# Kernel tuning notes

Measured on AMD Instinct MI355X. Metric: run time of the kernel, lower is better.

## Reference

```python
import jax, jax.numpy as jnp
import numpy as np

N, E, IN_F, EDGE_F, HID, S = 200000, 600000, 28, 4, 128, 20000
NUM_LAYERS = 4
L = NUM_LAYERS - 1
BN_EPS = 1e-5


def setup_inputs() -> dict:
    key = jax.random.key(0)
    ks = jax.random.split(key, 20)
    p = lambda k, shape: (jax.random.normal(k, shape, dtype=jnp.float32) * 0.1)
    return {
        'x': jax.random.normal(ks[0], (N, IN_F), dtype=jnp.float32),
        'edge_index': jax.random.randint(ks[1], (2, E), 0, N),
        'edge_attr': jax.random.normal(ks[2], (E, EDGE_F), dtype=jnp.float32),
        'edge_weight': jax.random.uniform(ks[3], (E,), dtype=jnp.float32),
        'node_mask': (jax.random.uniform(ks[4], (N,)) > 0.5).astype(jnp.float32),
        'subgraphs2nodes': jax.random.randint(ks[5], (N,), 0, S),
        # layer-1 params (in_features -> hidden)
        'be1_W1': p(ks[6], (EDGE_F, IN_F)), 'be1_b1': jnp.zeros((IN_F,), jnp.float32),
        'be1_W2': p(ks[7], (IN_F, IN_F)), 'be1_b2': jnp.zeros((IN_F,), jnp.float32),
        'm1_W1': p(ks[8], (IN_F, HID)), 'm1_b1': jnp.zeros((HID,), jnp.float32),
        'm1_W2': p(ks[9], (HID, HID)), 'm1_b2': jnp.zeros((HID,), jnp.float32),
        'bn1_g': jnp.ones((HID,), jnp.float32), 'bn1_b': jnp.zeros((HID,), jnp.float32),
        'eps1': jnp.zeros((), jnp.float32),
        # layers 2..NUM_LAYERS, stacked (hidden -> hidden)
        'beW1': p(ks[10], (L, EDGE_F, HID)), 'beb1': jnp.zeros((L, HID), jnp.float32),
        'beW2': p(ks[11], (L, HID, HID)), 'beb2': jnp.zeros((L, HID), jnp.float32),
        'mW1': p(ks[12], (L, HID, HID)), 'mb1': jnp.zeros((L, HID), jnp.float32),
        'mW2': p(ks[13], (L, HID, HID)), 'mb2': jnp.zeros((L, HID), jnp.float32),
        'bng': jnp.ones((L, HID), jnp.float32), 'bnb': jnp.zeros((L, HID), jnp.float32),
        'eps': jnp.zeros((L,), jnp.float32),
    }


def _mlp2(h, W1, b1, W2, b2):
    # Linear -> ReLU -> Linear
    return jnp.dot(jax.nn.relu(jnp.dot(h, W1) + b1), W2) + b2


def _gine(x, src, dst, edge_attr, edge_weight, eps,
          beW1, beb1, beW2, beb2, W1, b1, W2, b2, g, beta):
    # bond encoder on edge features
    e = _mlp2(edge_attr, beW1, beb1, beW2, beb2)            # [E, d]
    # message: relu(x_j + e_ij) * w_ij, aggregated at dst via scatter-add
    m = jax.nn.relu(x[src] + e) * edge_weight[:, None]      # [E, d]
    aggr = jax.ops.segment_sum(m, dst, num_segments=N)      # [N, d]
    h = (1.0 + eps) * x + aggr
    # node MLP: Linear,ReLU,Linear,BN(train mode),ReLU
    h = _mlp2(h, W1, b1, W2, b2)
    mu = jnp.mean(h, axis=0)
    var = jnp.mean((h - mu) ** 2, axis=0)
    h = (h - mu) * jax.lax.rsqrt(var + BN_EPS) * g + beta
    return jax.nn.relu(h)


def reference(x, edge_index, edge_attr, edge_weight, node_mask, subgraphs2nodes,
              be1_W1, be1_b1, be1_W2, be1_b2, m1_W1, m1_b1, m1_W2, m1_b2,
              bn1_g, bn1_b, eps1,
              beW1, beb1, beW2, beb2, mW1, mb1, mW2, mb2, bng, bnb, eps):
    src, dst = edge_index[0], edge_index[1]
    h = _gine(x, src, dst, edge_attr, edge_weight, eps1,
              be1_W1, be1_b1, be1_W2, be1_b2,
              m1_W1, m1_b1, m1_W2, m1_b2, bn1_g, bn1_b)
    for i in range(L):
        h_new = _gine(h, src, dst, edge_attr, edge_weight, eps[i],
                      beW1[i], beb1[i], beW2[i], beb2[i],
                      mW1[i], mb1[i], mW2[i], mb2[i], bng[i], bnb[i])
        h = h + h_new  # residual
    # float node_mask branch + global_add_pool over subgraphs2nodes
    h = h * node_mask[:, None]
    return jax.ops.segment_sum(h, subgraphs2nodes, num_segments=S)  # [S, HID]
```

## Files before the change

### kernel.cpp

```cpp
#include <hip/hip_runtime.h>
#include <hip/hip_bf16.h>


#define BNEPS 1e-5f
#define LDA 136
#define SCAN_NB 240

typedef __attribute__((ext_vector_type(8))) short bf16x8;
typedef __attribute__((ext_vector_type(8))) unsigned short u16x8;
typedef __attribute__((ext_vector_type(4))) float f32x4;

__device__ inline short f2bf(float f) {
    __hip_bfloat16 h = __float2bfloat16(f);
    return *reinterpret_cast<short*>(&h);
}
__device__ inline unsigned short f2bfu(float f) {
    __hip_bfloat16 h = __float2bfloat16(f);
    return *reinterpret_cast<unsigned short*>(&h);
}
__device__ inline float bf2f(unsigned short u) {
    union { unsigned int i; float f; } v; v.i = ((unsigned int)u) << 16; return v.f;
}

__global__ __launch_bounds__(256) void k_prep(
    const float* __restrict__ m1W2, const float* __restrict__ beW2,
    const float* __restrict__ mW1, const float* __restrict__ mW2,
    short* __restrict__ out)
{
    __shared__ float tileS[64][65];
    int b = blockIdx.x, mat = b >> 2, t = b & 3;
    const float* Wsrc;
    if (mat == 0) Wsrc = m1W2;
    else {
        int l = (mat - 1) / 3, which = (mat - 1) % 3;
        Wsrc = (which == 0) ? beW2 + (size_t)l * 16384
             : (which == 1) ? mW1 + (size_t)l * 16384
             :                mW2 + (size_t)l * 16384;
    }
    short* dst = out + (size_t)mat * 16384;
    int tr = (t >> 1) * 64, tc = (t & 1) * 64;
    for (int i = threadIdx.x; i < 4096; i += 256) {
        int r = i >> 6, c = i & 63;
        tileS[r][c] = Wsrc[(size_t)(tr + r) * 128 + (tc + c)];
    }
    __syncthreads();
    for (int i = threadIdx.x; i < 4096; i += 256) {
        int n = i >> 6, k = i & 63;
        dst[(size_t)(tc + n) * 128 + (tr + k)] = f2bf(tileS[k][n]);
    }
}

__global__ __launch_bounds__(256) void k_prep1(
    const float* __restrict__ W1, short* __restrict__ out)
{
    for (int i = threadIdx.x; i < 128 * 32; i += 256) {
        int n = i >> 5, k = i & 31;
        out[i] = (k < 28) ? f2bf(W1[(size_t)k * 128 + n]) : (short)0;
    }
}

__global__ __launch_bounds__(256) void k_prep28(
    const float* __restrict__ W2, short* __restrict__ out)
{
    for (int i = threadIdx.x; i < 32 * 32; i += 256) {
        int n = i >> 5, k = i & 31;
        out[i] = (n < 28 && k < 28) ? f2bf(W2[(size_t)k * 28 + n]) : (short)0;
    }
}

__global__ __launch_bounds__(256) void k_prepx(
    const float* __restrict__ x, unsigned short* __restrict__ xbf, int N)
{
    int total = N * 32;
    for (int i = blockIdx.x * 256 + threadIdx.x; i < total; i += gridDim.x * 256) {
        int n = i >> 5, c = i & 31;
        xbf[i] = (c < 28) ? f2bfu(x[(size_t)n * 28 + c]) : (unsigned short)0;
    }
}

__global__ __launch_bounds__(256) void k_count(
    const int* __restrict__ ei, int* __restrict__ counts, int E)
{
    for (int e = blockIdx.x * 256 + threadIdx.x; e < E; e += gridDim.x * 256)
        atomicAdd(&counts[ei[E + e]], 1);
}

__global__ __launch_bounds__(256) void k_count2(
    const int* __restrict__ s2n, const float* __restrict__ mask,
    int* __restrict__ counts2, int N)
{
    for (int n = blockIdx.x * 256 + threadIdx.x; n < N; n += gridDim.x * 256)
        if (mask[n] != 0.f) atomicAdd(&counts2[s2n[n]], 1);
}

__global__ __launch_bounds__(256) void k_scanA(
    const int* __restrict__ counts, int* __restrict__ bsum, int N, int seg)
{
    __shared__ int red[256];
    int b = blockIdx.x;
    int lo = b * seg, hi = min(lo + seg, N);
    int s = 0;
    for (int i = lo + threadIdx.x; i < hi; i += 256) s += counts[i];
    red[threadIdx.x] = s;
    __syncthreads();
    for (int d = 128; d > 0; d >>= 1) {
        if (threadIdx.x < d) red[threadIdx.x] += red[threadIdx.x + d];
        __syncthreads();
    }
    if (threadIdx.x == 0) bsum[b] = red[0];
}

__global__ __launch_bounds__(256) void k_scanB(
    int* __restrict__ bsum, int nb, int* __restrict__ offs, int N)
{
    __shared__ int sh[256];
    int v = (threadIdx.x < nb) ? bsum[threadIdx.x] : 0;
    sh[threadIdx.x] = v;
    __syncthreads();
    for (int d = 1; d < 256; d <<= 1) {
        int t = (threadIdx.x >= d) ? sh[threadIdx.x - d] : 0;
        __syncthreads();
        sh[threadIdx.x] += t;
        __syncthreads();
    }
    if (threadIdx.x < nb) bsum[threadIdx.x] = sh[threadIdx.x] - v;
    if (threadIdx.x == 0) offs[N] = sh[255];
}

__global__ __launch_bounds__(256) void k_scanC(
    const int* __restrict__ counts, const int* __restrict__ bsum,
    int* __restrict__ offs, int* __restrict__ cursor, int N, int seg)
{
    __shared__ int sh[256];
    int b = blockIdx.x;
    int lo = b * seg, hi = min(lo + seg, N);
    int base = bsum[b];
    for (int t0 = lo; t0 < hi; t0 += 256) {
        int i = t0 + threadIdx.x;
        int v = (i < hi) ? counts[i] : 0;
        sh[threadIdx.x] = v;
        __syncthreads();
        for (int d = 1; d < 256; d <<= 1) {
            int t = (threadIdx.x >= d) ? sh[threadIdx.x - d] : 0;
            __syncthreads();
            sh[threadIdx.x] += t;
            __syncthreads();
        }
        int excl = base + sh[threadIdx.x] - v;
        if (i < hi) { offs[i] = excl; cursor[i] = excl; }
        int tileTotal = sh[255];
        __syncthreads();
        base += tileTotal;
    }
}

__global__ __launch_bounds__(256) void k_scatter(
    const int* __restrict__ ei, const float* __restrict__ ew,
    const float4* __restrict__ ea4,
    int* __restrict__ cursor, int2* __restrict__ pmeta,
    float4* __restrict__ pea4, int E)
{
    for (int e = blockIdx.x * 256 + threadIdx.x; e < E; e += gridDim.x * 256) {
        int d = ei[E + e];
        int pos = atomicAdd(&cursor[d], 1);
        pmeta[pos] = make_int2(ei[e], __float_as_int(ew[e]));
        pea4[pos] = ea4[e];
    }
}

__global__ __launch_bounds__(256) void k_scatter2(
    const int* __restrict__ s2n, const float* __restrict__ mask,
    int* __restrict__ cursor2, int* __restrict__ perm2, int N)
{
    for (int n = blockIdx.x * 256 + threadIdx.x; n < N; n += gridDim.x * 256)
        if (mask[n] != 0.f) {
            int pos = atomicAdd(&cursor2[s2n[n]], 1);
            perm2[pos] = n;
        }
}

__global__ __launch_bounds__(256) void k_emsg(
    const float4* __restrict__ pea4,
    const float* __restrict__ W1, const float* __restrict__ b1,
    const short* __restrict__ W2t, const float* __restrict__ b2,
    unsigned short* __restrict__ emsg, const int* __restrict__ offs,
    int n0, int n1)
{
    __shared__ short Bs[128 * LDA];
    __shared__ short As[64 * LDA];
    __shared__ float eas[64][4];
    int e0 = offs[n0], e1 = offs[n1];
    int tid = threadIdx.x;
    for (int i = tid; i < 2048; i += 256) {
        int n = (i * 8) >> 7, k = (i * 8) & 127;
        *(bf16x8*)&Bs[n * LDA + k] = *(const bf16x8*)&W2t[i * 8];
    }
    int j = tid & 127, half = tid >> 7;
    float w10 = W1[j], w11 = W1[128 + j], w12 = W1[256 + j], w13 = W1[384 + j];
    float b1j = b1[j];
    int w = tid >> 6, lane = tid & 63;
    int l15 = lane & 15, quad = lane >> 4;
    __syncthreads();

    int numTiles = (e1 - e0 + 63) >> 6;
    for (int tile = blockIdx.x; tile < numTiles; tile += gridDim.x) {
        int base = e0 + tile * 64;
        __syncthreads();
        if (tid < 64) {
            int k = base + tid;
            float4 a = make_float4(0.f, 0.f, 0.f, 0.f);
            if (k < e1) a = pea4[k];
            eas[tid][0] = a.x; eas[tid][1] = a.y; eas[tid][2] = a.z; eas[tid][3] = a.w;
        }
        __syncthreads();
        #pragma unroll
        for (int q = 0; q < 32; ++q) {
            int e = half * 32 + q;
            float t = fmaf(eas[e][0], w10, fmaf(eas[e][1], w11,
                      fmaf(eas[e][2], w12, fmaf(eas[e][3], w13, b1j))));
            As[e * LDA + j] = f2bf(fmaxf(t, 0.f));
        }
        __syncthreads();
        f32x4 acc[8];
        #pragma unroll
        for (int nt = 0; nt < 8; ++nt) acc[nt] = (f32x4){0.f, 0.f, 0.f, 0.f};
        #pragma unroll
        for (int kt = 0; kt < 4; ++kt) {
            bf16x8 af = *(bf16x8*)&As[(w * 16 + l15) * LDA + kt * 32 + quad * 8];
            #pragma unroll
            for (int nt = 0; nt < 8; ++nt) {
                bf16x8 bf = *(bf16x8*)&Bs[(nt * 16 + l15) * LDA + kt * 32 + quad * 8];
                acc[nt] = __builtin_amdgcn_mfma_f32_16x16x32_bf16(af, bf, acc[nt], 0, 0, 0);
            }
        }
        #pragma unroll
        for (int nt = 0; nt < 8; ++nt) {
            int col = nt * 16 + l15;
            float b2c = b2[col];
            #pragma unroll
            for (int r = 0; r < 4; ++r) {
                int row = w * 16 + quad * 4 + r;
                As[row * LDA + col] = f2bf(acc[nt][r] + b2c);
            }
        }
        __syncthreads();
        #pragma unroll
        for (int kk = 0; kk < 4; ++kk) {
            int i = tid + kk * 256;
            int row = (i * 8) >> 7, col = (i * 8) & 127;
            int gr = base + row;
            if (gr < e1)
                *(bf16x8*)&emsg[(size_t)(gr - e0) * 128 + col] = *(bf16x8*)&As[row * LDA + col];
        }
    }
}

__global__ __launch_bounds__(256) void k_emsg28_mm(
    const float4* __restrict__ pea4,
    const float* __restrict__ W1, const float* __restrict__ b1,
    const short* __restrict__ W2t28,
    const float* __restrict__ b2,
    unsigned short* __restrict__ emsg28, int E)
{
    __shared__ short Bs[32 * 40];
    __shared__ short As[64 * 40];
    __shared__ float eas[64][4];
    __shared__ float b2s[32];
    int tid = threadIdx.x;
    for (int i = tid; i < 32 * 32; i += 256) {
        int n = i >> 5, k = i & 31;
        Bs[n * 40 + k] = W2t28[i];
    }
    if (tid < 32) b2s[tid] = (tid < 28) ? b2[tid] : 0.f;
    int j = tid & 31, sub = tid >> 5;
    float w10 = 0.f, w11 = 0.f, w12 = 0.f, w13 = 0.f, b1j = 0.f;
    if (j < 28) { w10 = W1[j]; w11 = W1[28 + j]; w12 = W1[56 + j]; w13 = W1[84 + j]; b1j = b1[j]; }
    int w = tid >> 6, lane = tid & 63;
    int l15 = lane & 15, quad = lane >> 4;
    __syncthreads();

    int numTiles = (E + 63) >> 6;
    for (int tile = blockIdx.x; tile < numTiles; tile += gridDim.x) {
        int base = tile * 64;
        __syncthreads();
        if (tid < 64) {
            int k = base + tid;
            float4 a = (k < E) ? pea4[k] : make_float4(0.f, 0.f, 0.f, 0.f);
            eas[tid][0] = a.x; eas[tid][1] = a.y; eas[tid][2] = a.z; eas[tid][3] = a.w;
        }
        __syncthreads();
        #pragma unroll
        for (int q = 0; q < 8; ++q) {
            int e = q * 8 + sub;
            float t = fmaf(eas[e][0], w10, fmaf(eas[e][1], w11,
                      fmaf(eas[e][2], w12, fmaf(eas[e][3], w13, b1j))));
            As[e * 40 + j] = (j < 28) ? f2bf(fmaxf(t, 0.f)) : (short)0;
        }
        __syncthreads();
        f32x4 acc[2];
        acc[0] = (f32x4){0.f, 0.f, 0.f, 0.f};
        acc[1] = (f32x4){0.f, 0.f, 0.f, 0.f};
        bf16x8 af = *(bf16x8*)&As[(w * 16 + l15) * 40 + quad * 8];
        #pragma unroll
        for (int nt = 0; nt < 2; ++nt) {
            bf16x8 bf = *(bf16x8*)&Bs[(nt * 16 + l15) * 40 + quad * 8];
            acc[nt] = __builtin_amdgcn_mfma_f32_16x16x32_bf16(af, bf, acc[nt], 0, 0, 0);
        }
        __syncthreads();
        #pragma unroll
        for (int nt = 0; nt < 2; ++nt) {
            int col = nt * 16 + l15;
            float bb = b2s[col];
            #pragma unroll
            for (int r = 0; r < 4; ++r)
                As[(w * 16 + quad * 4 + r) * 40 + col] = f2bf(acc[nt][r] + bb);
        }
        __syncthreads();
        for (int i = tid; i < 64 * 28; i += 256) {
            int row = i / 28, col = i - row * 28;
            int gr = base + row;
            if (gr < E) emsg28[(size_t)gr * 28 + col] = As[row * 40 + col];
        }
    }
}

__global__ __launch_bounds__(256) void k_gather(
    const unsigned short* __restrict__ h, const int* __restrict__ offs,
    const int2* __restrict__ pmeta, const unsigned short* __restrict__ emsg,
    unsigned short* __restrict__ a0,
    const float* __restrict__ epsp, int epsIdx,
    int n0, int n1)
{
    int grp = threadIdx.x >> 5, lane = threadIdx.x & 31;
    int n = n0 + blockIdx.x * 8 + grp;
    if (n >= n1) return;
    int e0 = offs[n0];
    int k0 = offs[n], k1 = offs[n + 1];
    float s = 1.0f + epsp[epsIdx];
    ushort4 hv0 = *(const ushort4*)&h[(size_t)n * 128 + lane * 4];
    float m0 = s * bf2f(hv0.x), m1 = s * bf2f(hv0.y);
    float m2 = s * bf2f(hv0.z), m3 = s * bf2f(hv0.w);
    for (int k = k0; k < k1; ++k) {
        int2 mt = pmeta[k];
        float w = __int_as_float(mt.y);
        ushort4 ev = *(const ushort4*)&emsg[(size_t)(k - e0) * 128 + lane * 4];
        ushort4 hv = *(const ushort4*)&h[(size_t)mt.x * 128 + lane * 4];
        m0 += fmaxf(bf2f(hv.x) + bf2f(ev.x), 0.f) * w;
        m1 += fmaxf(bf2f(hv.y) + bf2f(ev.y), 0.f) * w;
        m2 += fmaxf(bf2f(hv.z) + bf2f(ev.z), 0.f) * w;
        m3 += fmaxf(bf2f(hv.w) + bf2f(ev.w), 0.f) * w;
    }
    ushort4 o;
    o.x = f2bfu(m0); o.y = f2bfu(m1); o.z = f2bfu(m2); o.w = f2bfu(m3);
    *(ushort4*)&a0[(size_t)n * 128 + lane * 4] = o;
}

__global__ __launch_bounds__(256) void k_gather28(
    const float* __restrict__ x, const unsigned short* __restrict__ xbf,
    const int* __restrict__ offs,
    const int2* __restrict__ pmeta, const unsigned short* __restrict__ emsg28,
    const float* __restrict__ eps1, float* __restrict__ u28, int N)
{
    int grp = threadIdx.x >> 5, lane = threadIdx.x & 31;
    int n = blockIdx.x * 8 + grp;
    if (n >= N || lane >= 28) return;
    float s = 1.0f + eps1[0];
    int k0 = offs[n], k1 = offs[n + 1];
    float m = 0.f;
    for (int k = k0; k < k1; ++k) {
        int2 mt = pmeta[k];
        float w = __int_as_float(mt.y);
        float e = bf2f(emsg28[(size_t)k * 28 + lane]);
        float xs = bf2f(xbf[(size_t)mt.x * 32 + lane]);
        m += fmaxf(xs + e, 0.f) * w;
    }
    u28[(size_t)n * 28 + lane] = fmaf(s, x[(size_t)n * 28 + lane], m);
}

__global__ __launch_bounds__(512) void k_mlp(
    const unsigned short* __restrict__ src, const short* __restrict__ Wt1,
    const float* __restrict__ b1, const short* __restrict__ Wt2,
    const float* __restrict__ b2, unsigned short* __restrict__ dst,
    float* __restrict__ stats, int N)
{
    __shared__ short Bs1[128 * LDA];
    __shared__ short Bs2[128 * LDA];
    __shared__ short As[128 * LDA];
    __shared__ float sstat[256];
    int tid = threadIdx.x;
    for (int i = tid; i < 2048; i += 512) {
        int n = (i * 8) >> 7, k = (i * 8) & 127;
        *(bf16x8*)&Bs1[n * LDA + k] = *(const bf16x8*)&Wt1[i * 8];
        *(bf16x8*)&Bs2[n * LDA + k] = *(const bf16x8*)&Wt2[i * 8];
    }
    if (tid < 256) sstat[tid] = 0.f;
    int w = tid >> 6, lane = tid & 63;
    int l15 = lane & 15, quad = lane >> 4;
    int cg = w >> 2;
    int rb = (w & 3) * 32;
    __syncthreads();

    bf16x8 B1f[4][4], B2f[4][4];
    float b1r[4], b2r[4];
    #pragma unroll
    for (int nt = 0; nt < 4; ++nt) {
        int col = cg * 64 + nt * 16 + l15;
        b1r[nt] = b1[col]; b2r[nt] = b2[col];
        #pragma unroll
        for (int kt = 0; kt < 4; ++kt) {
            B1f[nt][kt] = *(bf16x8*)&Bs1[col * LDA + kt * 32 + quad * 8];
            B2f[nt][kt] = *(bf16x8*)&Bs2[col * LDA + kt * 32 + quad * 8];
        }
    }
    float lsum[2][4], lsq[2][4];
    #pragma unroll
    for (int rg = 0; rg < 2; ++rg)
        #pragma unroll
        for (int nt = 0; nt < 4; ++nt) { lsum[rg][nt] = 0.f; lsq[rg][nt] = 0.f; }

    int numTiles = (N + 127) >> 7;
    for (int tile = blockIdx.x; tile < numTiles; tile += gridDim.x) {
        int base = tile * 128;
        __syncthreads();
        #pragma unroll
        for (int kk = 0; kk < 4; ++kk) {
            int i = tid + kk * 512;
            int row = (i * 8) >> 7, col = (i * 8) & 127;
            int rr = base + row;
            bf16x8 v;
            if (rr < N) v = *(const bf16x8*)&src[(size_t)rr * 128 + col];
            else        v = (bf16x8){0,0,0,0,0,0,0,0};
            *(bf16x8*)&As[row * LDA + col] = v;
        }
        __syncthreads();
        f32x4 acc[2][4];
        #pragma unroll
        for (int rg = 0; rg < 2; ++rg)
            #pragma unroll
            for (int nt = 0; nt < 4; ++nt) acc[rg][nt] = (f32x4){0.f, 0.f, 0.f, 0.f};
        #pragma unroll
        for (int rg = 0; rg < 2; ++rg) {
            #pragma unroll
            for (int kt = 0; kt < 4; ++kt) {
                bf16x8 af = *(bf16x8*)&As[(rb + rg * 16 + l15) * LDA + kt * 32 + quad * 8];
                #pragma unroll
                for (int nt = 0; nt < 4; ++nt)
                    acc[rg][nt] = __builtin_amdgcn_mfma_f32_16x16x32_bf16(af, B1f[nt][kt], acc[rg][nt], 0, 0, 0);
            }
        }
        __syncthreads();
        #pragma unroll
        for (int rg = 0; rg < 2; ++rg)
            #pragma unroll
            for (int nt = 0; nt < 4; ++nt) {
                int col = cg * 64 + nt * 16 + l15;
                #pragma unroll
                for (int r = 0; r < 4; ++r)
                    As[(rb + rg * 16 + quad * 4 + r) * LDA + col] =
                        f2bf(fmaxf(acc[rg][nt][r] + b1r[nt], 0.f));
            }
        __syncthreads();
        #pragma unroll
        for (int rg = 0; rg < 2; ++rg)
            #pragma unroll
            for (int nt = 0; nt < 4; ++nt) acc[rg][nt] = (f32x4){0.f, 0.f, 0.f, 0.f};
        #pragma unroll
        for (int rg = 0; rg < 2; ++rg) {
            #pragma unroll
            for (int kt = 0; kt < 4; ++kt) {
                bf16x8 af = *(bf16x8*)&As[(rb + rg * 16 + l15) * LDA + kt * 32 + quad * 8];
                #pragma unroll
                for (int nt = 0; nt < 4; ++nt)
                    acc[rg][nt] = __builtin_amdgcn_mfma_f32_16x16x32_bf16(af, B2f[nt][kt], acc[rg][nt], 0, 0, 0);
            }
        }
        __syncthreads();
        #pragma unroll
        for (int rg = 0; rg < 2; ++rg)
            #pragma unroll
            for (int nt = 0; nt < 4; ++nt) {
                int col = cg * 64 + nt * 16 + l15;
                int row0 = base + rb + rg * 16 + quad * 4;
                #pragma unroll
                for (int r = 0; r < 4; ++r) {
                    float z = acc[rg][nt][r] + b2r[nt];
                    if (row0 + r < N) { lsum[rg][nt] += z; lsq[rg][nt] = fmaf(z, z, lsq[rg][nt]); }
                    As[(rb + rg * 16 + quad * 4 + r) * LDA + col] = f2bf(z);
                }
            }
        __syncthreads();
        #pragma unroll
        for (int kk = 0; kk < 4; ++kk) {
            int i = tid + kk * 512;
            int row = (i * 8) >> 7, col = (i * 8) & 127;
            int rr = base + row;
            if (rr < N)
                *(bf16x8*)&dst[(size_t)rr * 128 + col] = *(bf16x8*)&As[row * LDA + col];
        }
    }
    #pragma unroll
    for (int nt = 0; nt < 4; ++nt) {
        int col = cg * 64 + nt * 16 + l15;
        atomicAdd(&sstat[col], lsum[0][nt] + lsum[1][nt]);
        atomicAdd(&sstat[128 + col], lsq[0][nt] + lsq[1][nt]);
    }
    __syncthreads();
    if (tid < 256) atomicAdd(&stats[tid], sstat[tid]);
}

__global__ __launch_bounds__(512) void k_mlp1(
    const float* __restrict__ u28, const short* __restrict__ Wt1p,
    const float* __restrict__ b1, const short* __restrict__ Wt2,
    const float* __restrict__ b2, unsigned short* __restrict__ dst,
    float* __restrict__ stats, int N)
{
    __shared__ short Bs1[128 * 40];
    __shared__ short Bs2[128 * LDA];
    __shared__ short As[128 * LDA];
    __shared__ short A28[128 * 40];
    __shared__ float sstat[256];
    int tid = threadIdx.x;
    for (int i = tid; i < 128 * 32; i += 512) {
        int n = i >> 5, k = i & 31;
        Bs1[n * 40 + k] = Wt1p[i];
    }
    for (int i = tid; i < 2048; i += 512) {
        int n = (i * 8) >> 7, k = (i * 8) & 127;
        *(bf16x8*)&Bs2[n * LDA + k] = *(const bf16x8*)&Wt2[i * 8];
    }
    {
        int r = tid >> 2, c = tid & 3;
        if (r < 128) A28[r * 40 + 28 + c] = 0;
    }
    if (tid < 256) sstat[tid] = 0.f;
    int w = tid >> 6, lane = tid & 63;
    int l15 = lane & 15, quad = lane >> 4;
    int cg = w >> 2, rb = (w & 3) * 32;
    __syncthreads();

    bf16x8 B1f[4], B2f[4][4];
    float b1r[4], b2r[4];
    #pragma unroll
    for (int nt = 0; nt < 4; ++nt) {
        int col = cg * 64 + nt * 16 + l15;
        b1r[nt] = b1[col]; b2r[nt] = b2[col];
        B1f[nt] = *(bf16x8*)&Bs1[col * 40 + quad * 8];
        #pragma unroll
        for (int kt = 0; kt < 4; ++kt)
            B2f[nt][kt] = *(bf16x8*)&Bs2[col * LDA + kt * 32 + quad * 8];
    }
    float lsum[2][4], lsq[2][4];
    #pragma unroll
    for (int rg = 0; rg < 2; ++rg)
        #pragma unroll
        for (int nt = 0; nt < 4; ++nt) { lsum[rg][nt] = 0.f; lsq[rg][nt] = 0.f; }

    int numTiles = (N + 127) >> 7;
    for (int tile = blockIdx.x; tile < numTiles; tile += gridDim.x) {
        int base = tile * 128;
        __syncthreads();
        for (int i = tid; i < 128 * 28; i += 512) {
            int row = i / 28, col = i - row * 28;
            int rr = base + row;
            A28[row * 40 + col] = (rr < N) ? f2bf(u28[(size_t)rr * 28 + col]) : (short)0;
        }
        __syncthreads();
        f32x4 acc[2][4];
        #pragma unroll
        for (int rg = 0; rg < 2; ++rg)
            #pragma unroll
            for (int nt = 0; nt < 4; ++nt) acc[rg][nt] = (f32x4){0.f, 0.f, 0.f, 0.f};
        #pragma unroll
        for (int rg = 0; rg < 2; ++rg) {
            bf16x8 af = *(bf16x8*)&A28[(rb + rg * 16 + l15) * 40 + quad * 8];
            #pragma unroll
            for (int nt = 0; nt < 4; ++nt)
                acc[rg][nt] = __builtin_amdgcn_mfma_f32_16x16x32_bf16(af, B1f[nt], acc[rg][nt], 0, 0, 0);
        }
        #pragma unroll
        for (int rg = 0; rg < 2; ++rg)
            #pragma unroll
            for (int nt = 0; nt < 4; ++nt) {
                int col = cg * 64 + nt * 16 + l15;
                #pragma unroll
                for (int r = 0; r < 4; ++r)
                    As[(rb + rg * 16 + quad * 4 + r) * LDA + col] =
                        f2bf(fmaxf(acc[rg][nt][r] + b1r[nt], 0.f));
            }
        __syncthreads();
        #pragma unroll
        for (int rg = 0; rg < 2; ++rg)
            #pragma unroll
            for (int nt = 0; nt < 4; ++nt) acc[rg][nt] = (f32x4){0.f, 0.f, 0.f, 0.f};
        #pragma unroll
        for (int rg = 0; rg < 2; ++rg) {
            #pragma unroll
            for (int kt = 0; kt < 4; ++kt) {
                bf16x8 af = *(bf16x8*)&As[(rb + rg * 16 + l15) * LDA + kt * 32 + quad * 8];
                #pragma unroll
                for (int nt = 0; nt < 4; ++nt)
                    acc[rg][nt] = __builtin_amdgcn_mfma_f32_16x16x32_bf16(af, B2f[nt][kt], acc[rg][nt], 0, 0, 0);
            }
        }
        __syncthreads();
        #pragma unroll
        for (int rg = 0; rg < 2; ++rg)
            #pragma unroll
            for (int nt = 0; nt < 4; ++nt) {
                int col = cg * 64 + nt * 16 + l15;
                int row0 = base + rb + rg * 16 + quad * 4;
                #pragma unroll
                for (int r = 0; r < 4; ++r) {
                    float z = acc[rg][nt][r] + b2r[nt];
                    if (row0 + r < N) { lsum[rg][nt] += z; lsq[rg][nt] = fmaf(z, z, lsq[rg][nt]); }
                    As[(rb + rg * 16 + quad * 4 + r) * LDA + col] = f2bf(z);
                }
            }
        __syncthreads();
        #pragma unroll
        for (int kk = 0; kk < 4; ++kk) {
            int i = tid + kk * 512;
            int row = (i * 8) >> 7, col = (i * 8) & 127;
            int rr = base + row;
            if (rr < N)
                *(bf16x8*)&dst[(size_t)rr * 128 + col] = *(bf16x8*)&As[row * LDA + col];
        }
    }
    #pragma unroll
    for (int nt = 0; nt < 4; ++nt) {
        int col = cg * 64 + nt * 16 + l15;
        atomicAdd(&sstat[col], lsum[0][nt] + lsum[1][nt]);
        atomicAdd(&sstat[128 + col], lsq[0][nt] + lsq[1][nt]);
    }
    __syncthreads();
    if (tid < 256) atomicAdd(&stats[tid], sstat[tid]);
}

__global__ __launch_bounds__(128) void k_stats(
    const float* __restrict__ stats, const float* __restrict__ g,
    const float* __restrict__ b, float* __restrict__ ss, float invN)
{
    int j = threadIdx.x;
    float mu  = stats[j] * invN;
    float var = fmaf(stats[128 + j], invN, -mu * mu);
    float sc  = rsqrtf(fmaxf(var, 0.f) + BNEPS) * g[j];
    ss[j] = sc;
    ss[128 + j] = fmaf(-mu, sc, b[j]);
}

__global__ __launch_bounds__(256) void k_bn(
    const unsigned short* __restrict__ z, const float* __restrict__ ss,
    unsigned short* __restrict__ h, int residual, int N)
{
    int idx8 = blockIdx.x * 256 + threadIdx.x;
    int stride = gridDim.x * 256;
    int c0 = (idx8 & 15) * 8;
    float scl[8], sht[8];
    #pragma unroll
    for (int r = 0; r < 8; ++r) { scl[r] = ss[c0 + r]; sht[r] = ss[128 + c0 + r]; }
    int total8 = N * 16;
    for (; idx8 < total8; idx8 += stride) {
        int n = idx8 >> 4;
        u16x8 z8 = *(const u16x8*)&z[(size_t)n * 128 + c0];
        float hn[8];
        #pragma unroll
        for (int r = 0; r < 8; ++r)
            hn[r] = fmaxf(fmaf(bf2f(z8[r]), scl[r], sht[r]), 0.f);
        if (residual) {
            u16x8 h8 = *(const u16x8*)&h[(size_t)n * 128 + c0];
            #pragma unroll
            for (int r = 0; r < 8; ++r) hn[r] += bf2f(h8[r]);
        }
        u16x8 o;
        #pragma unroll
        for (int r = 0; r < 8; ++r) o[r] = f2bfu(hn[r]);
        *(u16x8*)&h[(size_t)n * 128 + c0] = o;
    }
}

__global__ __launch_bounds__(256) void k_poolbn(
    const unsigned short* __restrict__ z, const unsigned short* __restrict__ hprev,
    const float* __restrict__ ss, const int* __restrict__ offs2,
    const int* __restrict__ perm2, float* __restrict__ out, int S)
{
    int w = threadIdx.x >> 6, lane = threadIdx.x & 63;
    int s = blockIdx.x * 4 + w;
    if (s >= S) return;
    int c0 = lane * 2;
    float scl0 = ss[c0], scl1 = ss[c0 + 1];
    float sht0 = ss[128 + c0], sht1 = ss[128 + c0 + 1];
    int k0 = offs2[s], k1 = offs2[s + 1];
    float a0 = 0.f, a1 = 0.f;
    for (int k = k0; k < k1; ++k) {
        int n = perm2[k];
        ushort2 zv = *(const ushort2*)&z[(size_t)n * 128 + c0];
        ushort2 hv = *(const ushort2*)&hprev[(size_t)n * 128 + c0];
        a0 += fmaxf(fmaf(bf2f(zv.x), scl0, sht0), 0.f) + bf2f(hv.x);
        a1 += fmaxf(fmaf(bf2f(zv.y), scl1, sht1), 0.f) + bf2f(hv.y);
    }
    *(float2*)&out[(size_t)s * 128 + c0] = make_float2(a0, a1);
}

extern "C" void kernel_launch(void* const* d_in, const int* in_sizes, int n_in,
                              void* d_out, int out_size, void* d_ws, size_t ws_size,
                              hipStream_t stream) {
    const float* x    = (const float*)d_in[0];
    const int*   ei   = (const int*)d_in[1];
    const float* ea   = (const float*)d_in[2];
    const float* ew   = (const float*)d_in[3];
    const float* mask = (const float*)d_in[4];
    const int*   s2n  = (const int*)d_in[5];
    const float* be1W1 = (const float*)d_in[6];
    const float* be1b1 = (const float*)d_in[7];
    const float* be1W2 = (const float*)d_in[8];
    const float* be1b2 = (const float*)d_in[9];
    const float* m1W1  = (const float*)d_in[10];
    const float* m1b1  = (const float*)d_in[11];
    const float* m1W2  = (const float*)d_in[12];
    const float* m1b2  = (const float*)d_in[13];
    const float* bn1g  = (const float*)d_in[14];
    const float* bn1b  = (const float*)d_in[15];
    const float* eps1  = (const float*)d_in[16];
    const float* beW1  = (const float*)d_in[17];
    const float* beb1  = (const float*)d_in[18];
    const float* beW2  = (const float*)d_in[19];
    const float* beb2  = (const float*)d_in[20];
    const float* mW1   = (const float*)d_in[21];
    const float* mb1   = (const float*)d_in[22];
    const float* mW2   = (const float*)d_in[23];
    const float* mb2   = (const float*)d_in[24];
    const float* bng   = (const float*)d_in[25];
    const float* bnb   = (const float*)d_in[26];
    const float* epsL  = (const float*)d_in[27];

    const int N = in_sizes[0] / 28;
    const int E = in_sizes[1] / 2;
    const int S = out_size / 128;
    const float invN = 1.0f / (float)N;
    const int NS = N / 2;
    const int EMC = E / 2 + 8192;

    auto al16 = [](size_t v) { return (v + 15) & ~(size_t)15; };
    char* ws = (char*)d_ws;
    size_t offH      = 0;
    size_t offA0     = al16(offH + (size_t)N * 256);
    size_t offEm     = al16(offA0 + (size_t)N * 256);
    size_t emBytes   = (size_t)EMC * 256;
    if ((size_t)E * 56 > emBytes) emBytes = (size_t)E * 56;
    size_t offStats  = al16(offEm + emBytes);
    size_t offSS     = al16(offStats + 4096);
    size_t offWts    = al16(offSS + 1024);
    size_t offCounts = al16(offWts + 10 * 16384 * 2 + 4096 * 2 + 1024 * 2);
    size_t offOffs   = al16(offCounts + (size_t)N * 4);
    size_t offCursor = al16(offOffs + (size_t)(N + 1) * 4);
    size_t offPmeta  = al16(offCursor + (size_t)N * 4);
    size_t offPea    = al16(offPmeta + (size_t)E * 8);
    size_t offBsum   = al16(offPea + (size_t)E * 16);
    size_t offCnt2   = al16(offBsum + SCAN_NB * 4);
    size_t offOffs2  = al16(offCnt2 + (size_t)S * 4);
    size_t offCur2   = al16(offOffs2 + (size_t)(S + 1) * 4);
    size_t offPerm2  = al16(offCur2 + (size_t)S * 4);
    size_t need      = offPerm2 + (size_t)N * 4;
    if (ws_size < need) return;

    unsigned short* h    = (unsigned short*)(ws + offH);
    unsigned short* a0   = (unsigned short*)(ws + offA0);
    unsigned short* emsg = (unsigned short*)(ws + offEm);
    float* u28    = (float*)(ws + offA0);
    unsigned short* xbf = (unsigned short*)(ws + offA0 + 26214400);
    float* stats  = (float*)(ws + offStats);
    float* ssbuf  = (float*)(ws + offSS);
    short* wts    = (short*)(ws + offWts);
    short* w1p    = wts + 10 * 16384;
    short* w2p28  = w1p + 4096;
    int*   counts = (int*)(ws + offCounts);
    int*   offs   = (int*)(ws + offOffs);
    int*   cursor = (int*)(ws + offCursor);
    int2*  pmeta  = (int2*)(ws + offPmeta);
    float4* pea4  = (float4*)(ws + offPea);
    int*   bsum   = (int*)(ws + offBsum);
    int*   cnt2   = (int*)(ws + offCnt2);
    int*   offs2  = (int*)(ws + offOffs2);
    int*   cur2   = (int*)(ws + offCur2);
    int*   perm2  = (int*)(ws + offPerm2);
    const float4* ea4 = (const float4*)ea;

    hipMemsetAsync(stats, 0, 4 * 256 * sizeof(float), stream);
    hipMemsetAsync(counts, 0, (size_t)N * sizeof(int), stream);
    hipMemsetAsync(cnt2, 0, (size_t)S * sizeof(int), stream);

    k_prep<<<40, 256, 0, stream>>>(m1W2, beW2, mW1, mW2, wts);
    k_prep1<<<1, 256, 0, stream>>>(m1W1, w1p);
    k_prep28<<<1, 256, 0, stream>>>(be1W2, w2p28);
    k_prepx<<<512, 256, 0, stream>>>(x, xbf, N);

    const int seg = (N + SCAN_NB - 1) / SCAN_NB;
    k_count<<<1024, 256, 0, stream>>>(ei, counts, E);
    k_scanA<<<SCAN_NB, 256, 0, stream>>>(counts, bsum, N, seg);
    k_scanB<<<1, 256, 0, stream>>>(bsum, SCAN_NB, offs, N);
    k_scanC<<<SCAN_NB, 256, 0, stream>>>(counts, bsum, offs, cursor, N, seg);
    k_scatter<<<1024, 256, 0, stream>>>(ei, ew, ea4, cursor, pmeta, pea4, E);

    const int seg2 = (S + SCAN_NB - 1) / SCAN_NB;
    k_count2<<<512, 256, 0, stream>>>(s2n, mask, cnt2, N);
    k_scanA<<<SCAN_NB, 256, 0, stream>>>(cnt2, bsum, S, seg2);
    k_scanB<<<1, 256, 0, stream>>>(bsum, SCAN_NB, offs2, S);
    k_scanC<<<SCAN_NB, 256, 0, stream>>>(cnt2, bsum, offs2, cur2, S, seg2);
    k_scatter2<<<512, 256, 0, stream>>>(s2n, mask, cur2, perm2, N);

    auto wt_be = [&](int l) { return wts + (size_t)(1 + 3 * l + 0) * 16384; };
    auto wt_m1 = [&](int l) { return wts + (size_t)(1 + 3 * l + 1) * 16384; };
    auto wt_m2 = [&](int l) { return wts + (size_t)(1 + 3 * l + 2) * 16384; };

    k_emsg28_mm<<<2048, 256, 0, stream>>>(pea4, be1W1, be1b1, w2p28, be1b2, emsg, E);
    k_gather28<<<(N + 7) / 8, 256, 0, stream>>>(x, xbf, offs, pmeta, emsg, eps1, u28, N);
    k_mlp1<<<512, 512, 0, stream>>>(u28, w1p, m1b1, wts , m1b2, h, stats, N);
    k_stats<<<1, 128, 0, stream>>>(stats, bn1g, bn1b, ssbuf, invN);
    k_bn<<<2048, 256, 0, stream>>>(h, ssbuf, h, 0, N);

    for (int l = 0; l < 3; ++l) {
        for (int c = 0; c < 2; ++c) {
            int n0 = (c == 0) ? 0 : NS;
            int n1 = (c == 0) ? NS : N;
            k_emsg<<<2048, 256, 0, stream>>>(pea4,
                beW1 + (size_t)l * 512, beb1 + (size_t)l * 128,
                wt_be(l), beb2 + (size_t)l * 128, emsg, offs, n0, n1);
            k_gather<<<(n1 - n0 + 7) / 8, 256, 0, stream>>>(h, offs, pmeta, emsg, a0,
                epsL, l, n0, n1);
        }
        k_mlp<<<512, 512, 0, stream>>>(a0, wt_m1(l), mb1 + (size_t)l * 128,
                                       wt_m2(l), mb2 + (size_t)l * 128, a0,
                                       stats + 256 * (l + 1), N);
        k_stats<<<1, 128, 0, stream>>>(stats + 256 * (l + 1),
            bng + (size_t)l * 128, bnb + (size_t)l * 128, ssbuf, invN);
        if (l < 2) {
            k_bn<<<2048, 256, 0, stream>>>(a0, ssbuf, h, 1, N);
        }
    }

    k_poolbn<<<(S + 3) / 4, 256, 0, stream>>>(a0, h, ssbuf, offs2, perm2,
                                              (float*)d_out, S);
}
```

Baseline: 1.041 ms.

## Stream MLP weight fragments from global/L2 instead of LDS and registers

Removes the shared-memory copies of the weight matrices in k_emsg, k_mlp and k_mlp1 and stops holding all weight fragments in registers. Each k-step now loads its B fragments straight from global memory, relying on L2/L1 caching. Launch bounds now request 4 blocks per CU. The goal is less LDS use and fewer registers so more blocks fit per CU, at the cost of repeated global loads of the weights on every tile.

Result: slower. 1.785 ms (+71.5%).

```diff
diff --git a/kernel.cpp b/kernel.cpp
--- a/kernel.cpp
+++ b/kernel.cpp
@@ -179,28 +179,23 @@
         }
 }
 
-__global__ __launch_bounds__(256) void k_emsg(
+__global__ __launch_bounds__(256, 4) void k_emsg(
     const float4* __restrict__ pea4,
     const float* __restrict__ W1, const float* __restrict__ b1,
     const short* __restrict__ W2t, const float* __restrict__ b2,
     unsigned short* __restrict__ emsg, const int* __restrict__ offs,
     int n0, int n1)
 {
-    __shared__ short Bs[128 * LDA];
     __shared__ short As[64 * LDA];
     __shared__ float eas[64][4];
     int e0 = offs[n0], e1 = offs[n1];
     int tid = threadIdx.x;
-    for (int i = tid; i < 2048; i += 256) {
-        int n = (i * 8) >> 7, k = (i * 8) & 127;
-        *(bf16x8*)&Bs[n * LDA + k] = *(const bf16x8*)&W2t[i * 8];
-    }
     int j = tid & 127, half = tid >> 7;
     float w10 = W1[j], w11 = W1[128 + j], w12 = W1[256 + j], w13 = W1[384 + j];
     float b1j = b1[j];
     int w = tid >> 6, lane = tid & 63;
     int l15 = lane & 15, quad = lane >> 4;
-    __syncthreads();
+    const short* Wbase = W2t + (size_t)l15 * 128 + quad * 8;
 
     int numTiles = (e1 - e0 + 63) >> 6;
     for (int tile = blockIdx.x; tile < numTiles; tile += gridDim.x) {
@@ -226,13 +221,16 @@
         for (int nt = 0; nt < 8; ++nt) acc[nt] = (f32x4){0.f, 0.f, 0.f, 0.f};
         #pragma unroll
         for (int kt = 0; kt < 4; ++kt) {
+            bf16x8 bfr[8];
+            #pragma unroll
+            for (int nt = 0; nt < 8; ++nt)
+                bfr[nt] = *(const bf16x8*)&Wbase[nt * 16 * 128 + kt * 32];
             bf16x8 af = *(bf16x8*)&As[(w * 16 + l15) * LDA + kt * 32 + quad * 8];
             #pragma unroll
-            for (int nt = 0; nt < 8; ++nt) {
-                bf16x8 bf = *(bf16x8*)&Bs[(nt * 16 + l15) * LDA + kt * 32 + quad * 8];
-                acc[nt] = __builtin_amdgcn_mfma_f32_16x16x32_bf16(af, bf, acc[nt], 0, 0, 0);
-            }
-        }
+            for (int nt = 0; nt < 8; ++nt)
+                acc[nt] = __builtin_amdgcn_mfma_f32_16x16x32_bf16(af, bfr[nt], acc[nt], 0, 0, 0);
+        }
+        __syncthreads();
         #pragma unroll
         for (int nt = 0; nt < 8; ++nt) {
             int col = nt * 16 + l15;
@@ -377,46 +375,34 @@
     u28[(size_t)n * 28 + lane] = fmaf(s, x[(size_t)n * 28 + lane], m);
 }
 
-__global__ __launch_bounds__(512) void k_mlp(
+__global__ __launch_bounds__(512, 4) void k_mlp(
     const unsigned short* __restrict__ src, const short* __restrict__ Wt1,
     const float* __restrict__ b1, const short* __restrict__ Wt2,
     const float* __restrict__ b2, unsigned short* __restrict__ dst,
     float* __restrict__ stats, int N)
 {
-    __shared__ short Bs1[128 * LDA];
-    __shared__ short Bs2[128 * LDA];
     __shared__ short As[128 * LDA];
     __shared__ float sstat[256];
     int tid = threadIdx.x;
-    for (int i = tid; i < 2048; i += 512) {
-        int n = (i * 8) >> 7, k = (i * 8) & 127;
-        *(bf16x8*)&Bs1[n * LDA + k] = *(const bf16x8*)&Wt1[i * 8];
-        *(bf16x8*)&Bs2[n * LDA + k] = *(const bf16x8*)&Wt2[i * 8];
-    }
     if (tid < 256) sstat[tid] = 0.f;
     int w = tid >> 6, lane = tid & 63;
     int l15 = lane & 15, quad = lane >> 4;
     int cg = w >> 2;
     int rb = (w & 3) * 32;
-    __syncthreads();
-
-    bf16x8 B1f[4][4], B2f[4][4];
+    const short* W1base = Wt1 + (size_t)(cg * 64 + l15) * 128 + quad * 8;
+    const short* W2base = Wt2 + (size_t)(cg * 64 + l15) * 128 + quad * 8;
     float b1r[4], b2r[4];
     #pragma unroll
     for (int nt = 0; nt < 4; ++nt) {
         int col = cg * 64 + nt * 16 + l15;
         b1r[nt] = b1[col]; b2r[nt] = b2[col];
-        #pragma unroll
-        for (int kt = 0; kt < 4; ++kt) {
-            B1f[nt][kt] = *(bf16x8*)&Bs1[col * LDA + kt * 32 + quad * 8];
-            B2f[nt][kt] = *(bf16x8*)&Bs2[col * LDA + kt * 32 + quad * 8];
-        }
     }
     float lsum[2][4], lsq[2][4];
     #pragma unroll
     for (int rg = 0; rg < 2; ++rg)
         #pragma unroll
         for (int nt = 0; nt < 4; ++nt) { lsum[rg][nt] = 0.f; lsq[rg][nt] = 0.f; }
+    __syncthreads();
 
     int numTiles = (N + 127) >> 7;
     for (int tile = blockIdx.x; tile < numTiles; tile += gridDim.x) {
@@ -439,13 +425,17 @@
             #pragma unroll
             for (int nt = 0; nt < 4; ++nt) acc[rg][nt] = (f32x4){0.f, 0.f, 0.f, 0.f};
         #pragma unroll
-        for (int rg = 0; rg < 2; ++rg) {
-            #pragma unroll
-            for (int kt = 0; kt < 4; ++kt) {
+        for (int kt = 0; kt < 4; ++kt) {
+            bf16x8 b1f[4];
+            #pragma unroll
+            for (int nt = 0; nt < 4; ++nt)
+                b1f[nt] = *(const bf16x8*)&W1base[nt * 16 * 128 + kt * 32];
+            #pragma unroll
+            for (int rg = 0; rg < 2; ++rg) {
                 bf16x8 af = *(bf16x8*)&As[(rb + rg * 16 + l15) * LDA + kt * 32 + quad * 8];
                 #pragma unroll
                 for (int nt = 0; nt < 4; ++nt)
-                    acc[rg][nt] = __builtin_amdgcn_mfma_f32_16x16x32_bf16(af, B1f[nt][kt], acc[rg][nt], 0, 0, 0);
+                    acc[rg][nt] = __builtin_amdgcn_mfma_f32_16x16x32_bf16(af, b1f[nt], acc[rg][nt], 0, 0, 0);
             }
         }
         __syncthreads();
@@ -465,13 +455,17 @@
             #pragma unroll
             for (int nt = 0; nt < 4; ++nt) acc[rg][nt] = (f32x4){0.f, 0.f, 0.f, 0.f};
         #pragma unroll
-        for (int rg = 0; rg < 2; ++rg) {
-            #pragma unroll
-            for (int kt = 0; kt < 4; ++kt) {
+        for (int kt = 0; kt < 4; ++kt) {
+            bf16x8 b2f[4];
+            #pragma unroll
+            for (int nt = 0; nt < 4; ++nt)
+                b2f[nt] = *(const bf16x8*)&W2base[nt * 16 * 128 + kt * 32];
+            #pragma unroll
+            for (int rg = 0; rg < 2; ++rg) {
                 bf16x8 af = *(bf16x8*)&As[(rb + rg * 16 + l15) * LDA + kt * 32 + quad * 8];
                 #pragma unroll
                 for (int nt = 0; nt < 4; ++nt)
-                    acc[rg][nt] = __builtin_amdgcn_mfma_f32_16x16x32_bf16(af, B2f[nt][kt], acc[rg][nt], 0, 0, 0);
+                    acc[rg][nt] = __builtin_amdgcn_mfma_f32_16x16x32_bf16(af, b2f[nt], acc[rg][nt], 0, 0, 0);
             }
         }
         __syncthreads();
@@ -508,26 +502,16 @@
     if (tid < 256) atomicAdd(&stats[tid], sstat[tid]);
 }
 
-__global__ __launch_bounds__(512) void k_mlp1(
+__global__ __launch_bounds__(512, 4) void k_mlp1(
     const float* __restrict__ u28, const short* __restrict__ Wt1p,
     const float* __restrict__ b1, const short* __restrict__ Wt2,
     const float* __restrict__ b2, unsigned short* __restrict__ dst,
     float* __restrict__ stats, int N)
 {
-    __shared__ short Bs1[128 * 40];
-    __shared__ short Bs2[128 * LDA];
     __shared__ short As[128 * LDA];
     __shared__ short A28[128 * 40];
     __shared__ float sstat[256];
     int tid = threadIdx.x;
-    for (int i = tid; i < 128 * 32; i += 512) {
-        int n = i >> 5, k = i & 31;
-        Bs1[n * 40 + k] = Wt1p[i];
-    }
-    for (int i = tid; i < 2048; i += 512) {
-        int n = (i * 8) >> 7, k = (i * 8) & 127;
-        *(bf16x8*)&Bs2[n * LDA + k] = *(const bf16x8*)&Wt2[i * 8];
-    }
     {
         int r = tid >> 2, c = tid & 3;
         if (r < 128) A28[r * 40 + 28 + c] = 0;
@@ -536,24 +520,20 @@
     int w = tid >> 6, lane = tid & 63;
     int l15 = lane & 15, quad = lane >> 4;
     int cg = w >> 2, rb = (w & 3) * 32;
-    __syncthreads();
-
-    bf16x8 B1f[4], B2f[4][4];
+    const short* W1base = Wt1p + (size_t)(cg * 64 + l15) * 32 + quad * 8;
+    const short* W2base = Wt2 + (size_t)(cg * 64 + l15) * 128 + quad * 8;
     float b1r[4], b2r[4];
     #pragma unroll
     for (int nt = 0; nt < 4; ++nt) {
         int col = cg * 64 + nt * 16 + l15;
         b1r[nt] = b1[col]; b2r[nt] = b2[col];
-        B1f[nt] = *(bf16x8*)&Bs1[col * 40 + quad * 8];
-        #pragma unroll
-        for (int kt = 0; kt < 4; ++kt)
-            B2f[nt][kt] = *(bf16x8*)&Bs2[col * LDA + kt * 32 + quad * 8];
     }
     float lsum[2][4], lsq[2][4];
     #pragma unroll
     for (int rg = 0; rg < 2; ++rg)
         #pragma unroll
         for (int nt = 0; nt < 4; ++nt) { lsum[rg][nt] = 0.f; lsq[rg][nt] = 0.f; }
+    __syncthreads();
 
     int numTiles = (N + 127) >> 7;
     for (int tile = blockIdx.x; tile < numTiles; tile += gridDim.x) {
@@ -570,12 +550,18 @@
         for (int rg = 0; rg < 2; ++rg)
             #pragma unroll
             for (int nt = 0; nt < 4; ++nt) acc[rg][nt] = (f32x4){0.f, 0.f, 0.f, 0.f};
-        #pragma unroll
-        for (int rg = 0; rg < 2; ++rg) {
-            bf16x8 af = *(bf16x8*)&A28[(rb + rg * 16 + l15) * 40 + quad * 8];
+        {
+            bf16x8 b1f[4];
             #pragma unroll
             for (int nt = 0; nt < 4; ++nt)
-                acc[rg][nt] = __builtin_amdgcn_mfma_f32_16x16x32_bf16(af, B1f[nt], acc[rg][nt], 0, 0, 0);
+                b1f[nt] = *(const bf16x8*)&W1base[nt * 16 * 32];
+            #pragma unroll
+            for (int rg = 0; rg < 2; ++rg) {
+                bf16x8 af = *(bf16x8*)&A28[(rb + rg * 16 + l15) * 40 + quad * 8];
+                #pragma unroll
+                for (int nt = 0; nt < 4; ++nt)
+                    acc[rg][nt] = __builtin_amdgcn_mfma_f32_16x16x32_bf16(af, b1f[nt], acc[rg][nt], 0, 0, 0);
+            }
         }
         #pragma unroll
         for (int rg = 0; rg < 2; ++rg)
@@ -593,13 +579,17 @@
             #pragma unroll
             for (int nt = 0; nt < 4; ++nt) acc[rg][nt] = (f32x4){0.f, 0.f, 0.f, 0.f};
         #pragma unroll
-        for (int rg = 0; rg < 2; ++rg) {
-            #pragma unroll
-            for (int kt = 0; kt < 4; ++kt) {
+        for (int kt = 0; kt < 4; ++kt) {
+            bf16x8 b2f[4];
+            #pragma unroll
+            for (int nt = 0; nt < 4; ++nt)
+                b2f[nt] = *(const bf16x8*)&W2base[nt * 16 * 128 + kt * 32];
+            #pragma unroll
+            for (int rg = 0; rg < 2; ++rg) {
                 bf16x8 af = *(bf16x8*)&As[(rb + rg * 16 + l15) * LDA + kt * 32 + quad * 8];
                 #pragma unroll
                 for (int nt = 0; nt < 4; ++nt)
-                    acc[rg][nt] = __builtin_amdgcn_mfma_f32_16x16x32_bf16(af, B2f[nt][kt], acc[rg][nt], 0, 0, 0);
+                    acc[rg][nt] = __builtin_amdgcn_mfma_f32_16x16x32_bf16(af, b2f[nt], acc[rg][nt], 0, 0, 0);
             }
         }
         __syncthreads();
```
